# Optimization experiments

Hardware: AMD Instinct MI355X
Metric: run time of the kernel (lower is better)

## Reference

```python
import jax, jax.numpy as jnp
import numpy as np

C, N, E = 5, 50000, 800000   # relations (categories), nodes per category, edges per relation
DIN, H, DOUT = 128, 128, 64


def setup_inputs() -> dict:
    key = jax.random.key(0)
    ks = jax.random.split(key, 7)
    x = jax.random.normal(ks[0], (C, N, DIN), dtype=jnp.float32)
    edge_index = jax.random.randint(ks[1], (C, 2, E), 0, N)
    edge_weight = jax.random.uniform(ks[2], (C, E), dtype=jnp.float32, minval=0.1, maxval=1.0)
    W1 = jax.random.normal(ks[3], (C, DIN, H), dtype=jnp.float32) * (1.0 / np.sqrt(DIN))
    b1 = jnp.zeros((C, H), dtype=jnp.float32)
    W2 = jax.random.normal(ks[4], (C, H, DOUT), dtype=jnp.float32) * (1.0 / np.sqrt(H))
    b2 = jnp.zeros((C, DOUT), dtype=jnp.float32)
    return {"x": x, "edge_index": edge_index, "edge_weight": edge_weight,
            "W1": W1, "b1": b1, "W2": W2, "b2": b2}


def gcn_layer(x, src, dst, w, W, b):
    """PyG GCNConv: linear -> symmetric-normalized weighted scatter-add -> bias.
    Self-loops added with weight 1 (PyG default add_self_loops=True)."""
    n = x.shape[0]
    loop = jnp.arange(n)
    s = jnp.concatenate([src, loop])          # [E+N]
    d = jnp.concatenate([dst, loop])
    wa = jnp.concatenate([w, jnp.ones((n,), w.dtype)])
    deg = jax.ops.segment_sum(wa, d, num_segments=n)      # weighted in-degree (col)
    deg_safe = jnp.where(deg > 0, deg, 1.0)
    dis = jnp.where(deg > 0, jax.lax.rsqrt(deg_safe), 0.0)  # deg^-1/2, inf->0
    norm = dis[s] * wa * dis[d]                # [E+N]
    h = x @ W                                  # [N, F_out] transform before propagation
    msg = norm[:, None] * h[s]                 # gather + scale
    out = jnp.zeros((n, W.shape[1]), x.dtype).at[d].add(msg)  # scatter-add
    return out + b


def reference(x, edge_index, edge_weight, W1, b1, W2, b2):
    def per_relation(xc, ei, ew, w1, bb1, w2, bb2):
        h = jax.nn.relu(gcn_layer(xc, ei[0], ei[1], ew, w1, bb1))
        return gcn_layer(h, ei[0], ei[1], ew, w2, bb2)
    # Each node type receives from exactly one relation, so HeteroConv's 'sum'
    # aggregation is the identity; vmap over the 5 independent relations.
    return jax.vmap(per_relation)(x, edge_index, edge_weight, W1, b1, W2, b2)
```

## Files before the change

kernel.cpp:

```cpp
#include <hip/hip_runtime.h>
#include <hip/hip_fp16.h>

#define C_REL 5
#define NN    50000
#define EE    800000
#define D_IN  128
#define D_H   128
#define D_OUT 64

static constexpr int CN = C_REL * NN;
static constexpr int CE = C_REL * EE;
static constexpr int SCAN_B = (NN + 255) / 256;
static constexpr int BLK_GEMM_REL = (NN + 63) / 64;
static constexpr int BLK_AGG_REL  = NN / 4;
static constexpr int FILL_BLOCKS  = 2048;
static constexpr int FUSED_GRID   = 6144;

static constexpr unsigned long long MASK40 = (1ULL << 40) - 1;
static constexpr float FIX_SCALE = 16777216.0f;
static constexpr float FIX_INV   = 1.0f / 16777216.0f;

__device__ inline unsigned pack2h(float a, float b) {
  __half2 h = __floats2half2_rn(a, b);
  return *reinterpret_cast<unsigned*>(&h);
}


__global__ __launch_bounds__(256) void init_kernel(unsigned long long* packed) {
  int i = blockIdx.x * 256 + threadIdx.x;
  if (i < CN) packed[i] = 0ULL;
}

__global__ __launch_bounds__(256) void hist_kernel(const int* __restrict__ ei,
                                                   const float* __restrict__ ew,
                                                   unsigned long long* packed,
                                                   int* __restrict__ pos) {
  int stride = gridDim.x * 256;
  for (int idx = blockIdx.x * 256 + threadIdx.x; idx < CE; idx += stride) {
    int c = idx / EE, e = idx - c * EE;
    int d = ei[(c * 2 + 1) * EE + e];
    float w = ew[idx];
    unsigned long long wfix = (unsigned long long)(w * FIX_SCALE + 0.5f);
    unsigned long long old = atomicAdd(&packed[c * NN + d], (1ULL << 40) | wfix);
    pos[idx] = (int)(old >> 40);
  }
}

__global__ __launch_bounds__(256) void dis_kernel(const unsigned long long* __restrict__ packed,
                                                  float* __restrict__ dis) {
  int i = blockIdx.x * 256 + threadIdx.x;
  if (i >= CN) return;
  float deg = 1.0f + (float)(packed[i] & MASK40) * FIX_INV;
  dis[i] = rsqrtf(deg);
}

__global__ __launch_bounds__(256) void scan_a_kernel(const unsigned long long* __restrict__ packed,
                                                     int* rowptr, int* bsum) {
  int c = blockIdx.x / SCAN_B;
  int b = blockIdx.x - c * SCAN_B;
  int tid = threadIdx.x;
  int i = b * 256 + tid;
  int val = (i < NN) ? (int)(packed[c * NN + i] >> 40) : 0;
  __shared__ int sh[256];
  sh[tid] = val;
  __syncthreads();
  for (int off = 1; off < 256; off <<= 1) {
    int t = (tid >= off) ? sh[tid - off] : 0;
    __syncthreads();
    sh[tid] += t;
    __syncthreads();
  }
  if (i < NN) rowptr[c * (NN + 1) + i + 1] = sh[tid];
  if (tid == 255) bsum[c * 256 + b] = sh[255];
}

__global__ __launch_bounds__(256) void scan_b_kernel(int* bsum) {
  int c = blockIdx.x;
  int tid = threadIdx.x;
  int val = (tid < SCAN_B) ? bsum[c * 256 + tid] : 0;
  __shared__ int sh[256];
  sh[tid] = val;
  __syncthreads();
  for (int off = 1; off < 256; off <<= 1) {
    int t = (tid >= off) ? sh[tid - off] : 0;
    __syncthreads();
    sh[tid] += t;
    __syncthreads();
  }
  bsum[c * 256 + tid] = sh[tid] - val;
}

__global__ __launch_bounds__(256) void scan_c_kernel(int* rowptr, const int* __restrict__ bsum) {
  int c = blockIdx.x / SCAN_B;
  int b = blockIdx.x - c * SCAN_B;
  int i = b * 256 + threadIdx.x;
  if (i < NN) rowptr[c * (NN + 1) + i + 1] += bsum[c * 256 + b];
  if (i == 0) rowptr[c * (NN + 1)] = 0;
}


__device__ inline void fill_body(int bid, int nblocks,
                                 const int* __restrict__ ei,
                                 const float* __restrict__ ew,
                                 const float* __restrict__ dis,
                                 const int* __restrict__ rowptr,
                                 const int* __restrict__ pos,
                                 unsigned* __restrict__ csr) {
  int stride = nblocks * 256;
  for (int idx = bid * 256 + threadIdx.x; idx < CE; idx += stride) {
    int c = idx / EE, e = idx - c * EE;
    int s = ei[(c * 2 + 0) * EE + e];
    int d = ei[(c * 2 + 1) * EE + e];
    float w = ew[idx];
    float nrm = dis[c * NN + s] * w * dis[c * NN + d];
    int slot = rowptr[c * (NN + 1) + d] + pos[idx];
    unsigned ent = (unsigned)s | ((unsigned)__half_as_ushort(__float2half_rn(nrm)) << 16);
    csr[(size_t)c * EE + slot] = ent;
  }
}


template <int NC>
__device__ inline void gemm_body(int bid, const float* __restrict__ A,
                                 const float* __restrict__ B,
                                 __half* __restrict__ Cout) {
  constexpr int K = 128;
  constexpr int KC = 32;
  constexpr int CPT = NC / 32;
  __shared__ float Bs[K * NC];
  __shared__ float As[64][KC + 4];

  int c  = bid / BLK_GEMM_REL;
  int bl = bid - c * BLK_GEMM_REL;
  const float* Bc = B + (size_t)c * K * NC;
  const float* Ac = A + (size_t)c * NN * K;
  __half* Cc = Cout + (size_t)c * NN * NC;

  int tid = threadIdx.x;
  {
    const float4* B4 = (const float4*)Bc;
    float4* Bs4 = (float4*)Bs;
    for (int i = tid; i < K * NC / 4; i += 256) Bs4[i] = B4[i];
  }
  int tx = tid & 31;
  int ty = tid >> 5;
  int rowBase = bl * 64;

  float acc[8][CPT];
#pragma unroll
  for (int i = 0; i < 8; ++i)
#pragma unroll
    for (int j = 0; j < CPT; ++j) acc[i][j] = 0.f;

  for (int kc = 0; kc < K; kc += KC) {
    __syncthreads();
    int lr = tid >> 3;
    int lc = (tid & 7) * 4;
#pragma unroll
    for (int rr = 0; rr < 64; rr += 32) {
      int r = lr + rr;
      int gr = rowBase + r;
      float4 v = make_float4(0.f, 0.f, 0.f, 0.f);
      if (gr < NN) v = *(const float4*)&Ac[(size_t)gr * K + kc + lc];
      *(float4*)&As[r][lc] = v;
    }
    __syncthreads();

#pragma unroll
    for (int kk = 0; kk < KC; kk += 4) {
      float4 av[8];
#pragma unroll
      for (int i = 0; i < 8; ++i) av[i] = *(const float4*)&As[ty * 8 + i][kk];
#pragma unroll
      for (int u = 0; u < 4; ++u) {
        int k = kc + kk + u;
        if constexpr (CPT == 4) {
          float4 bv = *(const float4*)&Bs[k * NC + tx * 4];
#pragma unroll
          for (int i = 0; i < 8; ++i) {
            float a = ((const float*)&av[i])[u];
            acc[i][0] += a * bv.x;
            acc[i][1] += a * bv.y;
            acc[i][2] += a * bv.z;
            acc[i][3] += a * bv.w;
          }
        } else {
          float2 bv = *(const float2*)&Bs[k * NC + tx * 2];
#pragma unroll
          for (int i = 0; i < 8; ++i) {
            float a = ((const float*)&av[i])[u];
            acc[i][0] += a * bv.x;
            acc[i][1] += a * bv.y;
          }
        }
      }
    }
  }

#pragma unroll
  for (int i = 0; i < 8; ++i) {
    int gr = rowBase + ty * 8 + i;
    if (gr >= NN) continue;
    if constexpr (CPT == 4) {
      unsigned lo = pack2h(acc[i][0], acc[i][1]);
      unsigned hi = pack2h(acc[i][2], acc[i][3]);
      *(uint2*)&Cc[(size_t)gr * NC + tx * 4] = make_uint2(lo, hi);
    } else {
      *(unsigned*)&Cc[(size_t)gr * NC + tx * 2] = pack2h(acc[i][0], acc[i][1]);
    }
  }
}

__global__ __launch_bounds__(256) void fused_gemm1_fill_kernel(
    const float* __restrict__ x, const float* __restrict__ W1, __half* __restrict__ h1,
    const int* __restrict__ ei, const float* __restrict__ ew,
    const float* __restrict__ dis, const int* __restrict__ rowptr,
    const int* __restrict__ pos, unsigned* __restrict__ csr) {
  int id = blockIdx.x;
  int r = id % 3;
  if (r < 2) {
    int gid = (id / 3) * 2 + r;
    if (gid < C_REL * BLK_GEMM_REL) gemm_body<D_H>(gid, x, W1, h1);
  } else {
    fill_body(id / 3, FILL_BLOCKS, ei, ew, dis, rowptr, pos, csr);
  }
}

__global__ __launch_bounds__(256) void gemm2_kernel(const float* __restrict__ A,
                                                    const float* __restrict__ B,
                                                    __half* __restrict__ Cout) {
  gemm_body<D_OUT>(blockIdx.x, A, B, Cout);
}


__global__ __launch_bounds__(256) void agg1_kernel(const __half2* __restrict__ h,
                                                   const int* __restrict__ rowptr,
                                                   const unsigned* __restrict__ csr,
                                                   const float* __restrict__ dis,
                                                   const float* __restrict__ bias,
                                                   float* __restrict__ out) {
  int c  = blockIdx.x / BLK_AGG_REL;
  int bl = blockIdx.x - c * BLK_AGG_REL;
  int node = bl * 4 + (threadIdx.x >> 6);
  int lane = threadIdx.x & 63;

  const __half2* hc = h + (size_t)c * NN * 64;
  const unsigned* csrc = csr + (size_t)c * EE;
  int beg = rowptr[c * (NN + 1) + node];
  int end = rowptr[c * (NN + 1) + node + 1];

  float a0 = 0.f, a1 = 0.f;
  int idx = beg;
  for (; idx + 4 <= end; idx += 4) {
    unsigned e0 = csrc[idx], e1 = csrc[idx + 1], e2 = csrc[idx + 2], e3 = csrc[idx + 3];
    float2 v0 = __half22float2(hc[(size_t)(e0 & 0xffffu) * 64 + lane]);
    float2 v1 = __half22float2(hc[(size_t)(e1 & 0xffffu) * 64 + lane]);
    float2 v2 = __half22float2(hc[(size_t)(e2 & 0xffffu) * 64 + lane]);
    float2 v3 = __half22float2(hc[(size_t)(e3 & 0xffffu) * 64 + lane]);
    float n0 = __half2float(__ushort_as_half((unsigned short)(e0 >> 16)));
    float n1 = __half2float(__ushort_as_half((unsigned short)(e1 >> 16)));
    float n2 = __half2float(__ushort_as_half((unsigned short)(e2 >> 16)));
    float n3 = __half2float(__ushort_as_half((unsigned short)(e3 >> 16)));
    a0 += n0 * v0.x + n1 * v1.x + n2 * v2.x + n3 * v3.x;
    a1 += n0 * v0.y + n1 * v1.y + n2 * v2.y + n3 * v3.y;
  }
  for (; idx < end; ++idx) {
    unsigned e = csrc[idx];
    float2 v = __half22float2(hc[(size_t)(e & 0xffffu) * 64 + lane]);
    float nm = __half2float(__ushort_as_half((unsigned short)(e >> 16)));
    a0 += nm * v.x;
    a1 += nm * v.y;
  }
  float dn = dis[c * NN + node];
  float sn = dn * dn;
  float2 hv = __half22float2(hc[(size_t)node * 64 + lane]);
  int f = lane * 2;
  a0 += sn * hv.x + bias[c * 128 + f];
  a1 += sn * hv.y + bias[c * 128 + f + 1];
  a0 = fmaxf(a0, 0.f);
  a1 = fmaxf(a1, 0.f);
  *(float2*)&out[((size_t)c * NN + node) * 128 + f] = make_float2(a0, a1);
}


__global__ __launch_bounds__(256) void agg2_kernel(const __half2* __restrict__ h,
                                                   const int* __restrict__ rowptr,
                                                   const unsigned* __restrict__ csr,
                                                   const float* __restrict__ dis,
                                                   const float* __restrict__ bias,
                                                   float* __restrict__ out) {
  int c  = blockIdx.x / BLK_AGG_REL;
  int bl = blockIdx.x - c * BLK_AGG_REL;
  int node = bl * 4 + (threadIdx.x >> 6);
  int lane = threadIdx.x & 63;
  int hf = lane >> 5;
  int fl = lane & 31;

  const __half2* hc = h + (size_t)c * NN * 32;
  const unsigned* csrc = csr + (size_t)c * EE;
  int beg = rowptr[c * (NN + 1) + node];
  int end = rowptr[c * (NN + 1) + node + 1];

  float a0 = 0.f, a1 = 0.f;
  int idx = beg + hf;
  for (; idx + 2 < end; idx += 4) {
    unsigned ea = csrc[idx], eb = csrc[idx + 2];
    float2 va = __half22float2(hc[(size_t)(ea & 0xffffu) * 32 + fl]);
    float2 vb = __half22float2(hc[(size_t)(eb & 0xffffu) * 32 + fl]);
    float na = __half2float(__ushort_as_half((unsigned short)(ea >> 16)));
    float nb = __half2float(__ushort_as_half((unsigned short)(eb >> 16)));
    a0 += na * va.x + nb * vb.x;
    a1 += na * va.y + nb * vb.y;
  }
  for (; idx < end; idx += 2) {
    unsigned e = csrc[idx];
    float2 v = __half22float2(hc[(size_t)(e & 0xffffu) * 32 + fl]);
    float nm = __half2float(__ushort_as_half((unsigned short)(e >> 16)));
    a0 += nm * v.x;
    a1 += nm * v.y;
  }
  a0 += __shfl_xor(a0, 32, 64);
  a1 += __shfl_xor(a1, 32, 64);
  if (hf == 0) {
    float dn = dis[c * NN + node];
    float sn = dn * dn;
    float2 hv = __half22float2(hc[(size_t)node * 32 + fl]);
    int f = fl * 2;
    a0 += sn * hv.x + bias[c * 64 + f];
    a1 += sn * hv.y + bias[c * 64 + f + 1];
    *(float2*)&out[((size_t)c * NN + node) * 64 + f] = make_float2(a0, a1);
  }
}


extern "C" void kernel_launch(void* const* d_in, const int* in_sizes, int n_in,
                              void* d_out, int out_size, void* d_ws, size_t ws_size,
                              hipStream_t stream) {
  const float* x  = (const float*)d_in[0];
  const int*   ei = (const int*)d_in[1];
  const float* ew = (const float*)d_in[2];
  const float* W1 = (const float*)d_in[3];
  const float* b1 = (const float*)d_in[4];
  const float* W2 = (const float*)d_in[5];
  const float* b2 = (const float*)d_in[6];
  float* out = (float*)d_out;

  char* ws = (char*)d_ws;
  size_t off = 0;
  auto alloc = [&](size_t bytes) {
    size_t cur = off;
    off += (bytes + 255) & ~(size_t)255;
    return cur;
  };
  unsigned long long* packed = (unsigned long long*)(ws + alloc((size_t)CN * 8));
  float*    dis    = (float*)   (ws + alloc((size_t)CN * 4));
  int*      rowptr = (int*)     (ws + alloc((size_t)C_REL * (NN + 1) * 4));
  int*      bsum   = (int*)     (ws + alloc((size_t)C_REL * 256 * 4));
  unsigned* csr    = (unsigned*)(ws + alloc((size_t)CE * 4));
  __half*   h1     = (__half*)  (ws + alloc((size_t)CN * D_H * 2));
  float*    agg1   = (float*)   (ws + alloc((size_t)CN * D_H * 4));
  int* pos = (int*)agg1;

  const int NB_CN = (CN + 255) / 256;

  init_kernel<<<NB_CN, 256, 0, stream>>>(packed);
  hist_kernel<<<4096, 256, 0, stream>>>(ei, ew, packed, pos);
  dis_kernel<<<NB_CN, 256, 0, stream>>>(packed, dis);
  scan_a_kernel<<<C_REL * SCAN_B, 256, 0, stream>>>(packed, rowptr, bsum);
  scan_b_kernel<<<C_REL, 256, 0, stream>>>(bsum);
  scan_c_kernel<<<C_REL * SCAN_B, 256, 0, stream>>>(rowptr, bsum);

  fused_gemm1_fill_kernel<<<FUSED_GRID, 256, 0, stream>>>(x, W1, h1, ei, ew, dis,
                                                          rowptr, pos, csr);

  agg1_kernel<<<C_REL * BLK_AGG_REL, 256, 0, stream>>>((const __half2*)h1, rowptr, csr,
                                                       dis, b1, agg1);
  gemm2_kernel<<<C_REL * BLK_GEMM_REL, 256, 0, stream>>>(agg1, W2, h1);
  agg2_kernel<<<C_REL * BLK_AGG_REL, 256, 0, stream>>>((const __half2*)h1, rowptr, csr,
                                                       dis, b2, out);
}
```

Measured before the change: 843.4 us.

## Overlap gemm1 with histogram, store agg1 in fp16, chunk B tile in LDS

Moves the first dense transform so it runs alongside the atomic degree histogram in one fused launch, and makes the CSR fill a standalone kernel. The layer-1 aggregation output is stored as fp16 instead of fp32, and the second GEMM converts it back to fp32 while loading, halving that intermediate's traffic. The GEMM now stages only a 32-row slice of the weights in shared memory per K chunk, which reduces LDS use. The cost is extra rounding of the hidden activations and reloading weight slices on every chunk.

```diff
diff --git a/kernel.cpp b/kernel.cpp
--- a/kernel.cpp
+++ b/kernel.cpp
@@ -13,8 +13,10 @@
 static constexpr int SCAN_B = (NN + 255) / 256;
 static constexpr int BLK_GEMM_REL = (NN + 63) / 64;
 static constexpr int BLK_AGG_REL  = NN / 4;
-static constexpr int FILL_BLOCKS  = 2048;
-static constexpr int FUSED_GRID   = 6144;
+static constexpr int GEMM_BLOCKS  = C_REL * BLK_GEMM_REL;
+static constexpr int HIST_BLOCKS  = 4096;
+static constexpr int FUSED_GRID   = 2 * HIST_BLOCKS;
+static constexpr int FILL_BLOCKS  = 4096;
 
 static constexpr unsigned long long MASK40 = (1ULL << 40) - 1;
 static constexpr float FIX_SCALE = 16777216.0f;
@@ -31,12 +33,13 @@
   if (i < CN) packed[i] = 0ULL;
 }
 
-__global__ __launch_bounds__(256) void hist_kernel(const int* __restrict__ ei,
-                                                   const float* __restrict__ ew,
-                                                   unsigned long long* packed,
-                                                   int* __restrict__ pos) {
-  int stride = gridDim.x * 256;
-  for (int idx = blockIdx.x * 256 + threadIdx.x; idx < CE; idx += stride) {
+__device__ inline void hist_body(int bid, int nblocks,
+                                 const int* __restrict__ ei,
+                                 const float* __restrict__ ew,
+                                 unsigned long long* packed,
+                                 int* __restrict__ pos) {
+  int stride = nblocks * 256;
+  for (int idx = bid * 256 + threadIdx.x; idx < CE; idx += stride) {
     int c = idx / EE, e = idx - c * EE;
     int d = ei[(c * 2 + 1) * EE + e];
     float w = ew[idx];
@@ -98,16 +101,14 @@
   if (i == 0) rowptr[c * (NN + 1)] = 0;
 }
 
-
-__device__ inline void fill_body(int bid, int nblocks,
-                                 const int* __restrict__ ei,
-                                 const float* __restrict__ ew,
-                                 const float* __restrict__ dis,
-                                 const int* __restrict__ rowptr,
-                                 const int* __restrict__ pos,
-                                 unsigned* __restrict__ csr) {
-  int stride = nblocks * 256;
-  for (int idx = bid * 256 + threadIdx.x; idx < CE; idx += stride) {
+__global__ __launch_bounds__(256) void fill_kernel(const int* __restrict__ ei,
+                                                   const float* __restrict__ ew,
+                                                   const float* __restrict__ dis,
+                                                   const int* __restrict__ rowptr,
+                                                   const int* __restrict__ pos,
+                                                   unsigned* __restrict__ csr) {
+  int stride = gridDim.x * 256;
+  for (int idx = blockIdx.x * 256 + threadIdx.x; idx < CE; idx += stride) {
     int c = idx / EE, e = idx - c * EE;
     int s = ei[(c * 2 + 0) * EE + e];
     int d = ei[(c * 2 + 1) * EE + e];
@@ -120,28 +121,22 @@
 }
 
 
-template <int NC>
-__device__ inline void gemm_body(int bid, const float* __restrict__ A,
+template <int NC, bool AHALF>
+__device__ inline void gemm_body(int bid, const void* __restrict__ Av,
                                  const float* __restrict__ B,
                                  __half* __restrict__ Cout) {
   constexpr int K = 128;
   constexpr int KC = 32;
   constexpr int CPT = NC / 32;
-  __shared__ float Bs[K * NC];
+  __shared__ float Bs[KC * NC];
   __shared__ float As[64][KC + 4];
 
   int c  = bid / BLK_GEMM_REL;
   int bl = bid - c * BLK_GEMM_REL;
   const float* Bc = B + (size_t)c * K * NC;
-  const float* Ac = A + (size_t)c * NN * K;
   __half* Cc = Cout + (size_t)c * NN * NC;
 
   int tid = threadIdx.x;
-  {
-    const float4* B4 = (const float4*)Bc;
-    float4* Bs4 = (float4*)Bs;
-    for (int i = tid; i < K * NC / 4; i += 256) Bs4[i] = B4[i];
-  }
   int tx = tid & 31;
   int ty = tid >> 5;
   int rowBase = bl * 64;
@@ -154,15 +149,38 @@
 
   for (int kc = 0; kc < K; kc += KC) {
     __syncthreads();
-    int lr = tid >> 3;
-    int lc = (tid & 7) * 4;
-#pragma unroll
-    for (int rr = 0; rr < 64; rr += 32) {
-      int r = lr + rr;
-      int gr = rowBase + r;
-      float4 v = make_float4(0.f, 0.f, 0.f, 0.f);
-      if (gr < NN) v = *(const float4*)&Ac[(size_t)gr * K + kc + lc];
-      *(float4*)&As[r][lc] = v;
+    {
+      const float4* B4 = (const float4*)(Bc + (size_t)kc * NC);
+      float4* Bs4 = (float4*)Bs;
+#pragma unroll
+      for (int i = tid; i < KC * NC / 4; i += 256) Bs4[i] = B4[i];
+    }
+    if constexpr (AHALF) {
+      const __half* Ac = (const __half*)Av + (size_t)c * NN * K;
+      int lr = tid >> 2;
+      int lc = (tid & 3) * 8;
+      int gr = rowBase + lr;
+      uint4 v = make_uint4(0u, 0u, 0u, 0u);
+      if (gr < NN) v = *(const uint4*)&Ac[(size_t)gr * K + kc + lc];
+      const __half2* hp = (const __half2*)&v;
+#pragma unroll
+      for (int j = 0; j < 4; ++j) {
+        float2 f = __half22float2(hp[j]);
+        As[lr][lc + 2 * j]     = f.x;
+        As[lr][lc + 2 * j + 1] = f.y;
+      }
+    } else {
+      const float* Ac = (const float*)Av + (size_t)c * NN * K;
+      int lr = tid >> 3;
+      int lc = (tid & 7) * 4;
+#pragma unroll
+      for (int rr = 0; rr < 64; rr += 32) {
+        int r = lr + rr;
+        int gr = rowBase + r;
+        float4 v = make_float4(0.f, 0.f, 0.f, 0.f);
+        if (gr < NN) v = *(const float4*)&Ac[(size_t)gr * K + kc + lc];
+        *(float4*)&As[r][lc] = v;
+      }
     }
     __syncthreads();
 
@@ -173,7 +191,7 @@
       for (int i = 0; i < 8; ++i) av[i] = *(const float4*)&As[ty * 8 + i][kk];
 #pragma unroll
       for (int u = 0; u < 4; ++u) {
-        int k = kc + kk + u;
+        int k = kk + u;
         if constexpr (CPT == 4) {
           float4 bv = *(const float4*)&Bs[k * NC + tx * 4];
 #pragma unroll
@@ -211,25 +229,23 @@
   }
 }
 
-__global__ __launch_bounds__(256) void fused_gemm1_fill_kernel(
+__global__ __launch_bounds__(256) void fused_hist_gemm1_kernel(
     const float* __restrict__ x, const float* __restrict__ W1, __half* __restrict__ h1,
     const int* __restrict__ ei, const float* __restrict__ ew,
-    const float* __restrict__ dis, const int* __restrict__ rowptr,
-    const int* __restrict__ pos, unsigned* __restrict__ csr) {
+    unsigned long long* packed, int* __restrict__ pos) {
   int id = blockIdx.x;
-  int r = id % 3;
-  if (r < 2) {
-    int gid = (id / 3) * 2 + r;
-    if (gid < C_REL * BLK_GEMM_REL) gemm_body<D_H>(gid, x, W1, h1);
+  if (id & 1) {
+    hist_body(id >> 1, HIST_BLOCKS, ei, ew, packed, pos);
   } else {
-    fill_body(id / 3, FILL_BLOCKS, ei, ew, dis, rowptr, pos, csr);
-  }
-}
-
-__global__ __launch_bounds__(256) void gemm2_kernel(const float* __restrict__ A,
+    int gid = id >> 1;
+    if (gid < GEMM_BLOCKS) gemm_body<D_H, false>(gid, x, W1, h1);
+  }
+}
+
+__global__ __launch_bounds__(256) void gemm2_kernel(const __half* __restrict__ A,
                                                     const float* __restrict__ B,
                                                     __half* __restrict__ Cout) {
-  gemm_body<D_OUT>(blockIdx.x, A, B, Cout);
+  gemm_body<D_OUT, true>(blockIdx.x, A, B, Cout);
 }
 
 
@@ -238,7 +254,7 @@
                                                    const unsigned* __restrict__ csr,
                                                    const float* __restrict__ dis,
                                                    const float* __restrict__ bias,
-                                                   float* __restrict__ out) {
+                                                   __half* __restrict__ out) {
   int c  = blockIdx.x / BLK_AGG_REL;
   int bl = blockIdx.x - c * BLK_AGG_REL;
   int node = bl * 4 + (threadIdx.x >> 6);
@@ -279,7 +295,7 @@
   a1 += sn * hv.y + bias[c * 128 + f + 1];
   a0 = fmaxf(a0, 0.f);
   a1 = fmaxf(a1, 0.f);
-  *(float2*)&out[((size_t)c * NN + node) * 128 + f] = make_float2(a0, a1);
+  ((unsigned*)out)[((size_t)c * NN + node) * 64 + lane] = pack2h(a0, a1);
 }
 
 
@@ -358,24 +374,22 @@
   int*      bsum   = (int*)     (ws + alloc((size_t)C_REL * 256 * 4));
   unsigned* csr    = (unsigned*)(ws + alloc((size_t)CE * 4));
   __half*   h1     = (__half*)  (ws + alloc((size_t)CN * D_H * 2));
-  float*    agg1   = (float*)   (ws + alloc((size_t)CN * D_H * 4));
-  int* pos = (int*)agg1;
+  __half*   agg1h  = (__half*)  (ws + alloc((size_t)CN * D_H * 2));
+  int* pos = (int*)agg1h;
 
   const int NB_CN = (CN + 255) / 256;
 
   init_kernel<<<NB_CN, 256, 0, stream>>>(packed);
-  hist_kernel<<<4096, 256, 0, stream>>>(ei, ew, packed, pos);
+  fused_hist_gemm1_kernel<<<FUSED_GRID, 256, 0, stream>>>(x, W1, h1, ei, ew, packed, pos);
   dis_kernel<<<NB_CN, 256, 0, stream>>>(packed, dis);
   scan_a_kernel<<<C_REL * SCAN_B, 256, 0, stream>>>(packed, rowptr, bsum);
   scan_b_kernel<<<C_REL, 256, 0, stream>>>(bsum);
   scan_c_kernel<<<C_REL * SCAN_B, 256, 0, stream>>>(rowptr, bsum);
-
-  fused_gemm1_fill_kernel<<<FUSED_GRID, 256, 0, stream>>>(x, W1, h1, ei, ew, dis,
-                                                          rowptr, pos, csr);
+  fill_kernel<<<FILL_BLOCKS, 256, 0, stream>>>(ei, ew, dis, rowptr, pos, csr);
 
   agg1_kernel<<<C_REL * BLK_AGG_REL, 256, 0, stream>>>((const __half2*)h1, rowptr, csr,
-                                                       dis, b1, agg1);
-  gemm2_kernel<<<C_REL * BLK_GEMM_REL, 256, 0, stream>>>(agg1, W2, h1);
+                                                       dis, b1, agg1h);
+  gemm2_kernel<<<C_REL * BLK_GEMM_REL, 256, 0, stream>>>(agg1h, W2, h1);
   agg2_kernel<<<C_REL * BLK_AGG_REL, 256, 0, stream>>>((const __half2*)h1, rowptr, csr,
                                                        dis, b2, out);
 }
```

Result: faster. 726.3 us (-13.9%).
